# Optimization experiments

Measured on AMD Instinct MI355X. Metric: run time of the kernel, lower is better.

The kernel has to match this reference:

```python
import jax, jax.numpy as jnp
import numpy as np

N, C, H, W = 1, 1, 4096, 4096

def setup_inputs() -> dict:
    key = jax.random.key(0)
    x = jax.random.normal(key, (N, C, H, W), dtype=jnp.float32)
    return {"x": x}

def reference(x):
    # torch.median returns the lower of the two middle values for even counts:
    # take the k-th smallest with k = (n-1)//2.
    n = x.size
    median = jnp.sort(x.reshape(-1))[(n - 1) // 2]
    # threshold everything below the median to zero
    thresholded = jnp.where(x < median, jnp.float32(0.0), x)
    # 7x7 max pool, stride 1, padding 3 (torch pads with -inf for max pool)
    pooled = jax.lax.reduce_window(
        thresholded,
        -jnp.inf,
        jax.lax.max,
        window_dimensions=(1, 1, 7, 7),
        window_strides=(1, 1, 1, 1),
        padding=[(0, 0), (0, 0), (3, 3), (3, 3)],
    )
    # In the original, gather(flatten(thresholded), max_indices) == pooled,
    # so binarize where the thresholded value equals its local window max.
    binarized = jnp.where(thresholded == pooled, jnp.float32(1.0), jnp.float32(0.0))
    return binarized * x
```

## Files before the change

### kernel.cpp

```cpp
#include <hip/hip_runtime.h>
#include <math.h>

#define IMG_H 4096
#define IMG_W 4096
#define TS 64
#define HALO 3
#define TW 70
#define THS 71
#define HMS 65
#define NBINS 4096
#define CBLK 512
#define CAPA 2048
#define CAND_MAX (1u<<22)
#define WLO (-0.001953125f)
#define WHI ( 0.001953125f)
#define RSLOT 32
#define MCAP 1024
#define NSUB 2048

struct SelState {
    unsigned bin;
    unsigned k_rem;
    float    median;
    unsigned flag;
};

__device__ __forceinline__ unsigned f2u(float f) {
    unsigned b = __float_as_uint(f);
    unsigned mask = (unsigned)(-(int)(b >> 31)) | 0x80000000u;
    return b ^ mask;
}
__device__ __forceinline__ float u2f(unsigned u) {
    unsigned mask = (u >> 31) ? 0x80000000u : 0xFFFFFFFFu;
    return __uint_as_float(u ^ mask);
}

__device__ __forceinline__ int val_bin(float v) {
    float t = (v + 4.0f) * 512.0f;
    int b = (int)t;
    b = b < 0 ? 0 : b;
    b = b > (NBINS - 1) ? (NBINS - 1) : b;
    return b;
}

__device__ __forceinline__ int sub_bin(float v) {
    float t = (v - WLO) * (float)(NSUB * 256);
    int b = (int)t;
    b = b < 0 ? 0 : b;
    b = b > (NSUB - 1) ? (NSUB - 1) : b;
    return b;
}

__global__ __launch_bounds__(512) void count_compact(
    const float4* __restrict__ x4, int n4,
    unsigned* __restrict__ belowArr,
    unsigned* __restrict__ candA, unsigned* __restrict__ cntA)
{
    __shared__ unsigned buf[CAPA];
    __shared__ unsigned wred[8];
    __shared__ unsigned lcnt, gbase;
    const int t = threadIdx.x;
    if (t == 0) lcnt = 0;
    __syncthreads();

    unsigned below = 0;
    int idx = blockIdx.x * 512 + t;
    int stride = gridDim.x * 512;
    for (int i = idx; i < n4; i += stride) {
        float4 v = x4[i];
        float vs[4] = {v.x, v.y, v.z, v.w};
        #pragma unroll
        for (int j = 0; j < 4; j++) {
            float vv = vs[j];
            below += (vv < WLO) ? 1u : 0u;
            if (vv >= WLO && vv < WHI) {
                unsigned p = atomicAdd(&lcnt, 1u);
                unsigned key = f2u(vv);
                if (p < CAPA) buf[p] = key;
                else { unsigned q = atomicAdd(cntA, 1u); if (q < CAND_MAX) candA[q] = key; }
            }
        }
    }
    #pragma unroll
    for (int off = 32; off >= 1; off >>= 1) below += __shfl_down(below, off, 64);
    if ((t & 63) == 0) wred[t >> 6] = below;
    __syncthreads();
    if (t == 0) {
        unsigned tot = 0;
        #pragma unroll
        for (int w = 0; w < 8; w++) tot += wred[w];
        belowArr[blockIdx.x] = tot;
        gbase = atomicAdd(cntA, (lcnt > CAPA) ? CAPA : lcnt);
    }
    __syncthreads();
    unsigned m = lcnt; if (m > CAPA) m = CAPA;
    for (unsigned i = t; i < m; i += 512) {
        unsigned q = gbase + i;
        if (q < CAND_MAX) candA[q] = buf[i];
    }
}

__global__ __launch_bounds__(1024) void finalize_kernel(
    const unsigned* __restrict__ belowArr,
    const unsigned* __restrict__ candA, const unsigned* __restrict__ cntA,
    unsigned K, SelState* __restrict__ st)
{
    __shared__ unsigned hist[NSUB];
    __shared__ unsigned mem[MCAP];
    __shared__ unsigned wsum[16];
    __shared__ unsigned s_below, s_sb, s_kr2, mcnt;
    const int t = threadIdx.x;
    const unsigned lane = t & 63, wid = t >> 6;

    unsigned b = (t < CBLK) ? belowArr[t] : 0u;
    #pragma unroll
    for (int off = 32; off >= 1; off >>= 1) b += __shfl_down(b, off, 64);
    if (lane == 0) wsum[wid] = b;
    if (t == 0) mcnt = 0;
    __syncthreads();
    if (t == 0) {
        unsigned tot = 0;
        #pragma unroll
        for (int w = 0; w < 16; w++) tot += wsum[w];
        s_below = tot;
    }
    __syncthreads();

    const unsigned below = s_below;
    const unsigned M = *cntA;
    const bool direct = (K >= below) && (K - below < M) && (M <= RSLOT * 1024u);
    if (!direct) return;

    const unsigned kRem = K - below;

    unsigned rc[RSLOT];
    #pragma unroll
    for (int j = 0; j < RSLOT; j++) {
        int i = j * 1024 + t;
        rc[j] = (i < (int)M) ? candA[i] : 0u;
    }
    for (int i = t; i < NSUB; i += 1024) hist[i] = 0;
    __syncthreads();

    #pragma unroll
    for (int j = 0; j < RSLOT; j++) {
        int i = j * 1024 + t;
        if (i < (int)M) atomicAdd(&hist[sub_bin(u2f(rc[j]))], 1u);
    }
    __syncthreads();

    unsigned d0 = hist[t * 2], d1 = hist[t * 2 + 1];
    unsigned loc2 = d0 + d1;
    unsigned s2 = loc2;
    #pragma unroll
    for (int off = 1; off < 64; off <<= 1) {
        unsigned u = __shfl_up(s2, off, 64);
        if (lane >= off) s2 += u;
    }
    if (lane == 63) wsum[wid] = s2;
    __syncthreads();
    unsigned base2 = 0;
    for (unsigned w = 0; w < wid; w++) base2 += wsum[w];
    unsigned excl2 = base2 + s2 - loc2;
    if (kRem >= excl2 && kRem < excl2 + loc2) {
        if (kRem < excl2 + d0) { s_sb = (unsigned)(t * 2);     s_kr2 = kRem - excl2; }
        else                   { s_sb = (unsigned)(t * 2 + 1); s_kr2 = kRem - excl2 - d0; }
    }
    __syncthreads();

    const int sb = (int)s_sb;
    #pragma unroll
    for (int j = 0; j < RSLOT; j++) {
        int i = j * 1024 + t;
        if (i < (int)M && sub_bin(u2f(rc[j])) == sb) {
            unsigned p = atomicAdd(&mcnt, 1u);
            if (p < MCAP) mem[p] = rc[j];
        }
    }
    __syncthreads();
    if (mcnt > MCAP) return;

    const unsigned m = mcnt;
    const unsigned kr2 = s_kr2;
    if ((unsigned)t < m) {
        unsigned ku = mem[t];
        unsigned c = 0, e = 0;
        for (unsigned j = 0; j < m; j++) {
            unsigned kj = mem[j];
            c += (kj < ku);
            e += (kj == ku);
        }
        if (c <= kr2 && kr2 < c + e) { st->median = u2f(ku); st->flag = 1; }
    }
}


__global__ __launch_bounds__(256) void fb_hist(
    const float4* __restrict__ x4, int n4, const SelState* __restrict__ st,
    unsigned* __restrict__ gh)
{
    if (st->flag) return;
    __shared__ unsigned lh[NBINS];
    for (int i = threadIdx.x; i < NBINS; i += 256) lh[i] = 0;
    __syncthreads();
    int idx = blockIdx.x * 256 + threadIdx.x;
    int stride = gridDim.x * 256;
    for (int i = idx; i < n4; i += stride) {
        float4 v = x4[i];
        atomicAdd(&lh[val_bin(v.x)], 1u);
        atomicAdd(&lh[val_bin(v.y)], 1u);
        atomicAdd(&lh[val_bin(v.z)], 1u);
        atomicAdd(&lh[val_bin(v.w)], 1u);
    }
    __syncthreads();
    for (int i = threadIdx.x; i < NBINS; i += 256) {
        unsigned c = lh[i];
        if (c) atomicAdd(&gh[i], c);
    }
}

__global__ __launch_bounds__(1024) void fb_scan(
    const unsigned* __restrict__ gh, unsigned K, SelState* __restrict__ st)
{
    if (st->flag) return;
    __shared__ unsigned wsum[16];
    __shared__ unsigned s_bin, s_krem;
    const int t = threadIdx.x;
    const unsigned lane = t & 63, wid = t >> 6;
    unsigned cb[4];
    unsigned local = 0;
    #pragma unroll
    for (int j = 0; j < 4; j++) { cb[j] = gh[t * 4 + j]; local += cb[j]; }
    unsigned s = local;
    #pragma unroll
    for (int off = 1; off < 64; off <<= 1) {
        unsigned u = __shfl_up(s, off, 64);
        if (lane >= off) s += u;
    }
    if (lane == 63) wsum[wid] = s;
    __syncthreads();
    unsigned base = 0;
    for (unsigned w = 0; w < wid; w++) base += wsum[w];
    unsigned excl = base + s - local;
    if (K >= excl && K < excl + local) {
        unsigned cum = excl;
        #pragma unroll
        for (int j = 0; j < 4; j++) {
            if (K < cum + cb[j]) { s_bin = (unsigned)(t * 4 + j); s_krem = K - cum; break; }
            cum += cb[j];
        }
    }
    __syncthreads();
    if (t == 0) { st->bin = s_bin; st->k_rem = s_krem; }
}

__global__ __launch_bounds__(256) void fb_compact(
    const float4* __restrict__ x4, int n4, const SelState* __restrict__ st,
    unsigned* __restrict__ candB, unsigned* __restrict__ cntB)
{
    if (st->flag) return;
    __shared__ unsigned buf[CAPA];
    __shared__ unsigned lcnt, gbase;
    const int t = threadIdx.x;
    if (t == 0) lcnt = 0;
    __syncthreads();
    const int b = (int)st->bin;
    int idx = blockIdx.x * 256 + t;
    int stride = gridDim.x * 256;
    for (int i = idx; i < n4; i += stride) {
        float4 v = x4[i];
        float vs[4] = {v.x, v.y, v.z, v.w};
        #pragma unroll
        for (int j = 0; j < 4; j++) {
            if (val_bin(vs[j]) == b) {
                unsigned p = atomicAdd(&lcnt, 1u);
                if (p < CAPA) buf[p] = f2u(vs[j]);
                else { unsigned q = atomicAdd(cntB, 1u); candB[q] = f2u(vs[j]); }
            }
        }
    }
    __syncthreads();
    unsigned m = lcnt; if (m > CAPA) m = CAPA;
    if (t == 0) gbase = atomicAdd(cntB, m);
    __syncthreads();
    for (unsigned i = t; i < m; i += 256) candB[gbase + i] = buf[i];
}

__global__ __launch_bounds__(256) void fb_select(
    const unsigned* __restrict__ candB, const unsigned* __restrict__ cntB,
    SelState* __restrict__ st)
{
    if (st->flag) return;
    __shared__ unsigned hist[2048];
    __shared__ unsigned wsum[4];
    __shared__ unsigned s_pref, s_krem;
    const int t = threadIdx.x;
    const int M = (int)*cntB;
    if (t == 0) { s_pref = 0; s_krem = st->k_rem; }

    for (int p = 0; p < 3; p++) {
        const int shift = (p == 0) ? 21 : ((p == 1) ? 10 : 0);
        const int bits  = (p == 2) ? 10 : 11;
        const int nb    = 1 << bits;
        for (int i = t; i < nb; i += 256) hist[i] = 0;
        __syncthreads();
        const unsigned pref = s_pref;
        for (int i = t; i < M; i += 256) {
            unsigned u = candB[i];
            bool ok = (p == 0) || ((u >> ((p == 1) ? 21 : 10)) == pref);
            if (ok) atomicAdd(&hist[(u >> shift) & (unsigned)(nb - 1)], 1u);
        }
        __syncthreads();
        const int P = nb >> 8;
        unsigned cb[8];
        unsigned local = 0;
        for (int j = 0; j < P; j++) { cb[j] = hist[t * P + j]; local += cb[j]; }
        const unsigned lane = t & 63, wid = t >> 6;
        unsigned s = local;
        #pragma unroll
        for (int off = 1; off < 64; off <<= 1) {
            unsigned u = __shfl_up(s, off, 64);
            if (lane >= off) s += u;
        }
        if (lane == 63) wsum[wid] = s;
        __syncthreads();
        unsigned base = 0;
        for (unsigned w = 0; w < wid; w++) base += wsum[w];
        unsigned excl = base + s - local;
        unsigned kRem = s_krem;
        __syncthreads();
        if (kRem >= excl && kRem < excl + local) {
            unsigned cum = excl;
            for (int j = 0; j < P; j++) {
                if (kRem < cum + cb[j]) {
                    s_pref = (pref << bits) | (unsigned)(t * P + j);
                    s_krem = kRem - cum;
                    break;
                }
                cum += cb[j];
            }
        }
        __syncthreads();
    }
    if (t == 0) st->median = u2f(s_pref);
}

__global__ __launch_bounds__(512) void nms_kernel(
    const float* __restrict__ x, float* __restrict__ out,
    const SelState* __restrict__ st)
{
    __shared__ float th[TW * THS];
    __shared__ float hm[TW * HMS];

    const float med = st->median;
    const float NEGINF = -__builtin_inff();
    const int bx = blockIdx.x, by = blockIdx.y;
    const int gy0 = by * TS - HALO;
    const int gcol0 = bx * TS - 4;

    for (int task = threadIdx.x; task < TW * 18; task += 512) {
        int r = task / 18, q = task - r * 18;
        int gy = gy0 + r;
        int gxb = gcol0 + q * 4;
        bool rowok = (gy >= 0 && gy < IMG_H);
        float vs[4];
        if (rowok && gxb >= 0 && gxb + 4 <= IMG_W) {
            float4 v = *(const float4*)&x[gy * IMG_W + gxb];
            vs[0] = v.x; vs[1] = v.y; vs[2] = v.z; vs[3] = v.w;
        } else if (rowok) {
            #pragma unroll
            for (int cmp = 0; cmp < 4; cmp++) {
                int gx = gxb + cmp;
                vs[cmp] = (gx >= 0 && gx < IMG_W) ? x[gy * IMG_W + gx] : NEGINF;
            }
        } else {
            vs[0] = vs[1] = vs[2] = vs[3] = NEGINF;
        }
        #pragma unroll
        for (int cmp = 0; cmp < 4; cmp++) {
            int c = q * 4 - 1 + cmp;
            if ((unsigned)c < (unsigned)TW) {
                float v = vs[cmp];
                v = (v == NEGINF) ? v : ((v < med) ? 0.0f : v);
                th[r * THS + c] = v;
            }
        }
    }
    __syncthreads();

    for (int task = threadIdx.x; task < TW * 8; task += 512) {
        int r = task % TW;
        int c0 = (task / TW) * 8;
        float w[7];
        #pragma unroll
        for (int i = 0; i < 14; i++) {
            w[i % 7] = th[r * THS + c0 + i];
            if (i >= 6) {
                float m = w[0];
                #pragma unroll
                for (int k = 1; k < 7; k++) m = fmaxf(m, w[k]);
                hm[r * HMS + c0 + i - 6] = m;
            }
        }
    }
    __syncthreads();

    {
        const int c = threadIdx.x & 63;
        const int rr0 = (threadIdx.x >> 6) * 8;
        float w[7];
        #pragma unroll
        for (int i = 0; i < 14; i++) {
            w[i % 7] = hm[(rr0 + i) * HMS + c];
            if (i >= 6) {
                int R = rr0 + i - 6;
                float m = w[0];
                #pragma unroll
                for (int k = 1; k < 7; k++) m = fmaxf(m, w[k]);
                float t = th[(R + HALO) * THS + (c + HALO)];
                int gy = by * TS + R;
                int gx = bx * TS + c;
                float o = 0.0f;
                if (t == m) {
                    o = (t != 0.0f) ? t : x[gy * IMG_W + gx];
                }
                out[gy * IMG_W + gx] = o;
            }
        }
    }
}

extern "C" void kernel_launch(void* const* d_in, const int* in_sizes, int n_in,
                              void* d_out, int out_size, void* d_ws, size_t ws_size,
                              hipStream_t stream)
{
    const float* x = (const float*)d_in[0];
    float* out = (float*)d_out;
    const int n = in_sizes[0];
    const unsigned K = (unsigned)((n - 1) / 2);

    char* ws = (char*)d_ws;
    unsigned* gh       = (unsigned*)ws;
    unsigned* cntA     = (unsigned*)(ws + 16384);
    unsigned* cntB     = (unsigned*)(ws + 16388);
    SelState* st       = (SelState*)(ws + 16400);
    unsigned* belowArr = (unsigned*)(ws + 16640);
    unsigned* candA    = (unsigned*)(ws + ws_size / 2);

    hipMemsetAsync(d_ws, 0, 16416, stream);

    const int n4 = n / 4;
    count_compact<<<CBLK, 512, 0, stream>>>((const float4*)x, n4, belowArr, candA, cntA);
    finalize_kernel<<<1, 1024, 0, stream>>>(belowArr, candA, cntA, K, st);
    fb_hist<<<512, 256, 0, stream>>>((const float4*)x, n4, st, gh);
    fb_scan<<<1, 1024, 0, stream>>>(gh, K, st);
    fb_compact<<<512, 256, 0, stream>>>((const float4*)x, n4, st, (unsigned*)d_out, cntB);
    fb_select<<<1, 256, 0, stream>>>((const unsigned*)d_out, cntB, st);

    dim3 fg(IMG_W / TS, IMG_H / TS);
    nms_kernel<<<fg, 512, 0, stream>>>(x, out, st);
}
```

Measured before the change: 150.7 us.

## Merge fallback median kernels into one single-block exact kernel; double compaction blocks

Measured after the change: 149.2 us. Within noise of the previous version (-1.0%).

```diff
diff --git a/kernel.cpp b/kernel.cpp
--- a/kernel.cpp
+++ b/kernel.cpp
@@ -9,8 +9,8 @@
 #define THS 71
 #define HMS 65
 #define NBINS 4096
-#define CBLK 512
-#define CAPA 2048
+#define CBLK 1024
+#define CAPA 1024
 #define CAND_MAX (1u<<22)
 #define WLO (-0.001953125f)
 #define WHI ( 0.001953125f)
@@ -194,18 +194,20 @@
     }
 }
 
-
-__global__ __launch_bounds__(256) void fb_hist(
-    const float4* __restrict__ x4, int n4, const SelState* __restrict__ st,
-    unsigned* __restrict__ gh)
+__global__ __launch_bounds__(1024) void fb_exact(
+    const float4* __restrict__ x4, int n4, unsigned K,
+    unsigned* __restrict__ candB, SelState* __restrict__ st)
 {
     if (st->flag) return;
     __shared__ unsigned lh[NBINS];
-    for (int i = threadIdx.x; i < NBINS; i += 256) lh[i] = 0;
-    __syncthreads();
-    int idx = blockIdx.x * 256 + threadIdx.x;
-    int stride = gridDim.x * 256;
-    for (int i = idx; i < n4; i += stride) {
+    __shared__ unsigned wsum[16];
+    __shared__ unsigned s_bin, s_krem, s_m, s_pref, s_kr;
+    const int t = threadIdx.x;
+    const unsigned lane = t & 63, wid = t >> 6;
+
+    for (int i = t; i < NBINS; i += 1024) lh[i] = 0;
+    __syncthreads();
+    for (int i = t; i < n4; i += 1024) {
         float4 v = x4[i];
         atomicAdd(&lh[val_bin(v.x)], 1u);
         atomicAdd(&lh[val_bin(v.y)], 1u);
@@ -213,109 +215,72 @@
         atomicAdd(&lh[val_bin(v.w)], 1u);
     }
     __syncthreads();
-    for (int i = threadIdx.x; i < NBINS; i += 256) {
-        unsigned c = lh[i];
-        if (c) atomicAdd(&gh[i], c);
-    }
-}
-
-__global__ __launch_bounds__(1024) void fb_scan(
-    const unsigned* __restrict__ gh, unsigned K, SelState* __restrict__ st)
-{
-    if (st->flag) return;
-    __shared__ unsigned wsum[16];
-    __shared__ unsigned s_bin, s_krem;
-    const int t = threadIdx.x;
-    const unsigned lane = t & 63, wid = t >> 6;
-    unsigned cb[4];
-    unsigned local = 0;
-    #pragma unroll
-    for (int j = 0; j < 4; j++) { cb[j] = gh[t * 4 + j]; local += cb[j]; }
-    unsigned s = local;
-    #pragma unroll
-    for (int off = 1; off < 64; off <<= 1) {
-        unsigned u = __shfl_up(s, off, 64);
-        if (lane >= off) s += u;
-    }
-    if (lane == 63) wsum[wid] = s;
-    __syncthreads();
-    unsigned base = 0;
-    for (unsigned w = 0; w < wid; w++) base += wsum[w];
-    unsigned excl = base + s - local;
-    if (K >= excl && K < excl + local) {
-        unsigned cum = excl;
-        #pragma unroll
-        for (int j = 0; j < 4; j++) {
-            if (K < cum + cb[j]) { s_bin = (unsigned)(t * 4 + j); s_krem = K - cum; break; }
-            cum += cb[j];
-        }
-    }
-    __syncthreads();
-    if (t == 0) { st->bin = s_bin; st->k_rem = s_krem; }
-}
-
-__global__ __launch_bounds__(256) void fb_compact(
-    const float4* __restrict__ x4, int n4, const SelState* __restrict__ st,
-    unsigned* __restrict__ candB, unsigned* __restrict__ cntB)
-{
-    if (st->flag) return;
-    __shared__ unsigned buf[CAPA];
-    __shared__ unsigned lcnt, gbase;
-    const int t = threadIdx.x;
-    if (t == 0) lcnt = 0;
-    __syncthreads();
-    const int b = (int)st->bin;
-    int idx = blockIdx.x * 256 + t;
-    int stride = gridDim.x * 256;
-    for (int i = idx; i < n4; i += stride) {
-        float4 v = x4[i];
-        float vs[4] = {v.x, v.y, v.z, v.w};
-        #pragma unroll
-        for (int j = 0; j < 4; j++) {
-            if (val_bin(vs[j]) == b) {
-                unsigned p = atomicAdd(&lcnt, 1u);
-                if (p < CAPA) buf[p] = f2u(vs[j]);
-                else { unsigned q = atomicAdd(cntB, 1u); candB[q] = f2u(vs[j]); }
-            }
-        }
-    }
-    __syncthreads();
-    unsigned m = lcnt; if (m > CAPA) m = CAPA;
-    if (t == 0) gbase = atomicAdd(cntB, m);
-    __syncthreads();
-    for (unsigned i = t; i < m; i += 256) candB[gbase + i] = buf[i];
-}
-
-__global__ __launch_bounds__(256) void fb_select(
-    const unsigned* __restrict__ candB, const unsigned* __restrict__ cntB,
-    SelState* __restrict__ st)
-{
-    if (st->flag) return;
-    __shared__ unsigned hist[2048];
-    __shared__ unsigned wsum[4];
-    __shared__ unsigned s_pref, s_krem;
-    const int t = threadIdx.x;
-    const int M = (int)*cntB;
-    if (t == 0) { s_pref = 0; s_krem = st->k_rem; }
-
+
+    {
+        unsigned cb[4];
+        unsigned local = 0;
+        #pragma unroll
+        for (int j = 0; j < 4; j++) { cb[j] = lh[t * 4 + j]; local += cb[j]; }
+        unsigned s = local;
+        #pragma unroll
+        for (int off = 1; off < 64; off <<= 1) {
+            unsigned u = __shfl_up(s, off, 64);
+            if (lane >= off) s += u;
+        }
+        if (lane == 63) wsum[wid] = s;
+        __syncthreads();
+        unsigned base = 0;
+        for (unsigned w = 0; w < wid; w++) base += wsum[w];
+        unsigned excl = base + s - local;
+        if (K >= excl && K < excl + local) {
+            unsigned cum = excl;
+            #pragma unroll
+            for (int j = 0; j < 4; j++) {
+                if (K < cum + cb[j]) { s_bin = (unsigned)(t * 4 + j); s_krem = K - cum; break; }
+                cum += cb[j];
+            }
+        }
+        if (t == 0) s_m = 0;
+        __syncthreads();
+    }
+
+    {
+        const int b = (int)s_bin;
+        for (int i = t; i < n4; i += 1024) {
+            float4 v = x4[i];
+            float vs[4] = {v.x, v.y, v.z, v.w};
+            #pragma unroll
+            for (int j = 0; j < 4; j++) {
+                if (val_bin(vs[j]) == b) {
+                    unsigned p = atomicAdd(&s_m, 1u);
+                    candB[p] = f2u(vs[j]);
+                }
+            }
+        }
+        __syncthreads();
+    }
+
+    const int M = (int)s_m;
+    if (t == 0) { s_pref = 0; s_kr = s_krem; }
     for (int p = 0; p < 3; p++) {
         const int shift = (p == 0) ? 21 : ((p == 1) ? 10 : 0);
         const int bits  = (p == 2) ? 10 : 11;
         const int nb    = 1 << bits;
-        for (int i = t; i < nb; i += 256) hist[i] = 0;
+        for (int i = t; i < nb; i += 1024) lh[i] = 0;
         __syncthreads();
         const unsigned pref = s_pref;
-        for (int i = t; i < M; i += 256) {
+        for (int i = t; i < M; i += 1024) {
             unsigned u = candB[i];
             bool ok = (p == 0) || ((u >> ((p == 1) ? 21 : 10)) == pref);
-            if (ok) atomicAdd(&hist[(u >> shift) & (unsigned)(nb - 1)], 1u);
-        }
-        __syncthreads();
-        const int P = nb >> 8;
-        unsigned cb[8];
-        unsigned local = 0;
-        for (int j = 0; j < P; j++) { cb[j] = hist[t * P + j]; local += cb[j]; }
-        const unsigned lane = t & 63, wid = t >> 6;
+            if (ok) atomicAdd(&lh[(u >> shift) & (unsigned)(nb - 1)], 1u);
+        }
+        __syncthreads();
+        const int P = nb >> 10;
+        unsigned c0 = lh[t * (P ? P : 1)];
+        unsigned c1 = (P == 2) ? lh[t * 2 + 1] : 0u;
+        unsigned valid = (P >= 1) || (t < nb);
+        if (P == 0) { c0 = (t < nb) ? lh[t] : 0u; c1 = 0u; }
+        unsigned local = valid ? (c0 + c1) : 0u;
         unsigned s = local;
         #pragma unroll
         for (int off = 1; off < 64; off <<= 1) {
@@ -327,17 +292,15 @@
         unsigned base = 0;
         for (unsigned w = 0; w < wid; w++) base += wsum[w];
         unsigned excl = base + s - local;
-        unsigned kRem = s_krem;
+        unsigned kRem = s_kr;
         __syncthreads();
         if (kRem >= excl && kRem < excl + local) {
-            unsigned cum = excl;
-            for (int j = 0; j < P; j++) {
-                if (kRem < cum + cb[j]) {
-                    s_pref = (pref << bits) | (unsigned)(t * P + j);
-                    s_krem = kRem - cum;
-                    break;
-                }
-                cum += cb[j];
+            if (P == 2) {
+                if (kRem < excl + c0) { s_pref = (pref << bits) | (unsigned)(t * 2);     s_kr = kRem - excl; }
+                else                  { s_pref = (pref << bits) | (unsigned)(t * 2 + 1); s_kr = kRem - excl - c0; }
+            } else {
+                s_pref = (pref << bits) | (unsigned)t;
+                s_kr = kRem - excl;
             }
         }
         __syncthreads();
@@ -440,22 +403,17 @@
     const unsigned K = (unsigned)((n - 1) / 2);
 
     char* ws = (char*)d_ws;
-    unsigned* gh       = (unsigned*)ws;
-    unsigned* cntA     = (unsigned*)(ws + 16384);
-    unsigned* cntB     = (unsigned*)(ws + 16388);
-    SelState* st       = (SelState*)(ws + 16400);
-    unsigned* belowArr = (unsigned*)(ws + 16640);
+    unsigned* cntA     = (unsigned*)ws;
+    SelState* st       = (SelState*)(ws + 16);
+    unsigned* belowArr = (unsigned*)(ws + 256);
     unsigned* candA    = (unsigned*)(ws + ws_size / 2);
 
-    hipMemsetAsync(d_ws, 0, 16416, stream);
+    hipMemsetAsync(d_ws, 0, 32, stream);
 
     const int n4 = n / 4;
     count_compact<<<CBLK, 512, 0, stream>>>((const float4*)x, n4, belowArr, candA, cntA);
     finalize_kernel<<<1, 1024, 0, stream>>>(belowArr, candA, cntA, K, st);
-    fb_hist<<<512, 256, 0, stream>>>((const float4*)x, n4, st, gh);
-    fb_scan<<<1, 1024, 0, stream>>>(gh, K, st);
-    fb_compact<<<512, 256, 0, stream>>>((const float4*)x, n4, st, (unsigned*)d_out, cntB);
-    fb_select<<<1, 256, 0, stream>>>((const unsigned*)d_out, cntB, st);
+    fb_exact<<<1, 1024, 0, stream>>>((const float4*)x, n4, K, (unsigned*)d_out, st);
 
     dim3 fg(IMG_W / TS, IMG_H / TS);
     nms_kernel<<<fg, 512, 0, stream>>>(x, out, st);
```
